# Kernel tuning notes

Hardware: AMD Instinct MI355X
Metric: run time of the kernel (lower is better)

The kernel has to match this reference:

```python
import jax, jax.numpy as jnp
import numpy as np

NEG = -9e15

def setup_inputs() -> dict:
    key = jax.random.key(0)
    k1, k2, k3, k4, k5 = jax.random.split(key, 5)
    N, Fin, Fout = 8192, 256, 128
    h = jax.random.normal(k1, (N, Fin), dtype=jnp.float32)
    adj = jax.random.randint(k2, (N, N), 0, 2, dtype=jnp.int32)
    # Parameters (xavier_uniform with gain=1.414 for a1/a2; kaiming-like for W is fine as random init)
    lim_w = float(np.sqrt(6.0 / (Fin + Fout)))
    W = jax.random.uniform(k3, (Fout, Fin), dtype=jnp.float32, minval=-lim_w, maxval=lim_w)
    lim_a = float(1.414 * np.sqrt(6.0 / (Fout + 1)))
    a1 = jax.random.uniform(k4, (Fout, 1), dtype=jnp.float32, minval=-lim_a, maxval=lim_a)
    a2 = jax.random.uniform(k5, (Fout, 1), dtype=jnp.float32, minval=-lim_a, maxval=lim_a)
    return {"h": h, "adj": adj, "W": W, "a1": a1, "a2": a2}

def reference(h, adj, W, a1, a2):
    Wh = h @ W.T                                   # [N, Fout]
    s1 = (Wh @ a1)                                 # [N, 1]
    s2 = (Wh @ a2)                                 # [N, 1]
    e = jax.nn.leaky_relu(s1 + s2.T, 0.2)          # [N, N]
    att = jnp.where(adj > 0, e, jnp.float32(NEG))
    att = jax.nn.softmax(att, axis=1)
    h_prime = att @ Wh                             # [N, Fout]
    return jax.nn.elu(h_prime)
```

## Files before the change

### kernel.cpp

```cpp
#include <hip/hip_runtime.h>
#include <cstdint>
#include <cstddef>

#define N_NODES 8192
#define FIN 256
#define FOUT 128
#define MT 32
#define KC 256
#define JS 4
#define JW (N_NODES / JS)
#define NCHS (JW / KC)
#define LOG2E 1.4426950408889634f

typedef __attribute__((ext_vector_type(8))) short bf16x8;
typedef __attribute__((ext_vector_type(4))) float f32x4;
typedef __attribute__((ext_vector_type(4))) int i32x4;
typedef __attribute__((ext_vector_type(2))) unsigned int u32x2;
typedef __attribute__((ext_vector_type(4))) unsigned int u32x4;

__device__ __forceinline__ float bf2f(unsigned short u) {
    union { unsigned int i; float f; } v; v.i = ((unsigned int)u) << 16; return v.f;
}
__device__ __forceinline__ unsigned short f2bf(float f) {
    union { float f; unsigned int i; } v; v.f = f;
    unsigned int r = (v.i + 0x7FFFu + ((v.i >> 16) & 1u)) >> 16;
    return (unsigned short)r;
}
__device__ __forceinline__ unsigned int pack_bf16(float a, float b) {
    return (unsigned)f2bf(a) | ((unsigned)f2bf(b) << 16);
}

__device__ __forceinline__ size_t whb_idx(int j, int f) {
    return ((size_t)((j >> 5) * 8 + (f >> 4)) << 9) + (((j >> 3) & 3) << 7)
         + ((f & 15) << 3) + (j & 7);
}

__global__ __launch_bounds__(256) void wh_kernel(const float* __restrict__ h,
                                                 const float* __restrict__ W,
                                                 const float* __restrict__ a1,
                                                 const float* __restrict__ a2,
                                                 unsigned short* __restrict__ whB,
                                                 float* __restrict__ s1p,
                                                 float* __restrict__ s2p) {
    __shared__ float hT[64][FIN + 5];
    __shared__ float p1[4][64], p2[4][64];
    const int t = threadIdx.x;
    const int i0 = blockIdx.x * 64;
    const int f0 = blockIdx.y * 32;
#pragma unroll
    for (int c = 0; c < 16; ++c) {
        int chunk = c * 256 + t;
        int row = chunk >> 6, col = (chunk & 63) * 4;
        f32x4 v = *(const f32x4*)&h[(size_t)(i0 + row) * FIN + col];
        hT[row][col] = v[0]; hT[row][col + 1] = v[1];
        hT[row][col + 2] = v[2]; hT[row][col + 3] = v[3];
    }
    __syncthreads();
    const int lane = t & 63;
    const int wv = t >> 6;
    const int fb8 = __builtin_amdgcn_readfirstlane(f0 + wv * 8);
    const float* w0 = W + (size_t)fb8 * FIN;
    float acc[8] = {0.f, 0.f, 0.f, 0.f, 0.f, 0.f, 0.f, 0.f};
    for (int k = 0; k < FIN; k += 4) {
        float h0 = hT[lane][k],     h1 = hT[lane][k + 1];
        float h2 = hT[lane][k + 2], h3 = hT[lane][k + 3];
#pragma unroll
        for (int c = 0; c < 8; ++c) {
            const float* wr = w0 + c * FIN;
            acc[c] += h0 * wr[k] + h1 * wr[k + 1] + h2 * wr[k + 2] + h3 * wr[k + 3];
        }
    }
    const int i = i0 + lane;
    float sp1 = 0.f, sp2 = 0.f;
#pragma unroll
    for (int c = 0; c < 8; ++c) {
        whB[whb_idx(i, fb8 + c)] = f2bf(acc[c]);
        sp1 += acc[c] * a1[fb8 + c];
        sp2 += acc[c] * a2[fb8 + c];
    }
    p1[wv][lane] = sp1; p2[wv][lane] = sp2;
    __syncthreads();
    if (t < 64) {
        float v1 = (p1[0][lane] + p1[1][lane]) + (p1[2][lane] + p1[3][lane]);
        float v2 = (p2[0][lane] + p2[1][lane]) + (p2[2][lane] + p2[3][lane]);
        s1p[(size_t)blockIdx.y * N_NODES + i0 + lane] = v1 * LOG2E;
        s2p[(size_t)blockIdx.y * N_NODES + i0 + lane] = v2 * LOG2E;
    }
}

__global__ __launch_bounds__(256) void gat_kernel(const int* __restrict__ adj,
                                                  const unsigned short* __restrict__ whB,
                                                  const float* __restrict__ s1p,
                                                  const float* __restrict__ s2p,
                                                  float* __restrict__ out,
                                                  float* __restrict__ nums,
                                                  float* __restrict__ dens) {
    __shared__ __align__(16) unsigned short sP[MT][KC + 8];
    __shared__ __align__(16) float sS2[JW / 1];
    __shared__ float sDen[MT];
    __shared__ float sS1[MT];
    const int t = threadIdx.x;
    const int slice = blockIdx.x & (JS - 1);
    const int i0 = (blockIdx.x >> 2) * MT;
    const int jb = slice * JW;
    const int kb0 = slice * (JW / 32);
    float* __restrict__ num = slice ? (nums + (size_t)(slice - 1) * N_NODES * FOUT) : out;
    float* __restrict__ den = dens + (size_t)slice * N_NODES;

    {
        const float* p0 = s2p + jb + t * 8;
        f32x4 a = {0.f, 0.f, 0.f, 0.f}, b = {0.f, 0.f, 0.f, 0.f};
#pragma unroll
        for (int pb = 0; pb < 4; ++pb) {
            a += *(const f32x4*)(p0 + (size_t)pb * N_NODES);
            b += *(const f32x4*)(p0 + (size_t)pb * N_NODES + 4);
        }
        *(f32x4*)&sS2[t * 8]     = a;
        *(f32x4*)&sS2[t * 8 + 4] = b;
    }
    if (t < MT) {
        float a = 0.f;
#pragma unroll
        for (int pb = 0; pb < 4; ++pb) a += s1p[(size_t)pb * N_NODES + i0 + t];
        sS1[t] = a;
        sDen[t] = 0.f;
    }
    __syncthreads();

    const int r0 = t >> 4;
    const int s  = t & 15;
    const int lane = t & 63;
    const int quad = lane >> 4;
    const int sl = lane & 15;
    const int wv = t >> 6;
    const int* __restrict__ aRow0 = adj + (size_t)(i0 + r0) * N_NODES + jb;
    const int* __restrict__ aRow1 = aRow0 + (size_t)16 * N_NODES;
    const float s1a = sS1[r0];
    const float s1b = sS1[r0 + 16];

    f32x4 acc00 = {0.f,0.f,0.f,0.f}, acc01 = {0.f,0.f,0.f,0.f};
    f32x4 acc10 = {0.f,0.f,0.f,0.f}, acc11 = {0.f,0.f,0.f,0.f};

    for (int ch = 0; ch < NCHS; ++ch) {
        const int cb = ch * KC + s * 16;
        i32x4 av0[4], av1[4];
        f32x4 sv[4];
#pragma unroll
        for (int q = 0; q < 4; ++q) {
            av0[q] = *(const i32x4*)&aRow0[cb + q * 4];
            av1[q] = *(const i32x4*)&aRow1[cb + q * 4];
            sv[q]  = *(const f32x4*)&sS2[cb + q * 4];
        }
        float part0 = 0.f, part1 = 0.f;
        unsigned int w0[8], w1[8];
#pragma unroll
        for (int q = 0; q < 4; ++q) {
            float p0[4], p1v[4];
#pragma unroll
            for (int r = 0; r < 4; ++r) {
                float y0 = s1a + sv[q][r];
                float y1 = s1b + sv[q][r];
                y0 = fmaxf(y0, 0.2f * y0);
                y1 = fmaxf(y1, 0.2f * y1);
                float e0 = __builtin_amdgcn_exp2f(y0);
                float e1 = __builtin_amdgcn_exp2f(y1);
                p0[r]  = (av0[q][r] > 0) ? e0 : 0.f;
                p1v[r] = (av1[q][r] > 0) ? e1 : 0.f;
                part0 += p0[r];
                part1 += p1v[r];
            }
            w0[2 * q]     = pack_bf16(p0[0], p0[1]);
            w0[2 * q + 1] = pack_bf16(p0[2], p0[3]);
            w1[2 * q]     = pack_bf16(p1v[0], p1v[1]);
            w1[2 * q + 1] = pack_bf16(p1v[2], p1v[3]);
        }
        u32x4 ra = {w0[0], w0[1], w0[2], w0[3]};
        u32x4 rb = {w0[4], w0[5], w0[6], w0[7]};
        u32x4 rc = {w1[0], w1[1], w1[2], w1[3]};
        u32x4 rd = {w1[4], w1[5], w1[6], w1[7]};
        *(u32x4*)&sP[r0][s * 16]          = ra;
        *(u32x4*)&sP[r0][s * 16 + 8]      = rb;
        *(u32x4*)&sP[r0 + 16][s * 16]     = rc;
        *(u32x4*)&sP[r0 + 16][s * 16 + 8] = rd;
        part0 += __shfl_xor(part0, 1); part1 += __shfl_xor(part1, 1);
        part0 += __shfl_xor(part0, 2); part1 += __shfl_xor(part1, 2);
        part0 += __shfl_xor(part0, 4); part1 += __shfl_xor(part1, 4);
        part0 += __shfl_xor(part0, 8); part1 += __shfl_xor(part1, 8);
        if (s == 0) { sDen[r0] += part0; sDen[r0 + 16] += part1; }
        __syncthreads();
#pragma unroll
        for (int kq = 0; kq < KC / 32; ++kq) {
            bf16x8 a0  = *(const bf16x8*)&sP[sl][kq * 32 + quad * 8];
            bf16x8 a1f = *(const bf16x8*)&sP[16 + sl][kq * 32 + quad * 8];
            int kb = kb0 + ch * (KC / 32) + kq;
            const unsigned short* t0 = whB + ((size_t)(kb * 8 + wv * 2) << 9) + lane * 8;
            bf16x8 b0 = *(const bf16x8*)t0;
            bf16x8 b1 = *(const bf16x8*)(t0 + 512);
            acc00 = __builtin_amdgcn_mfma_f32_16x16x32_bf16(a0,  b0, acc00, 0, 0, 0);
            acc01 = __builtin_amdgcn_mfma_f32_16x16x32_bf16(a0,  b1, acc01, 0, 0, 0);
            acc10 = __builtin_amdgcn_mfma_f32_16x16x32_bf16(a1f, b0, acc10, 0, 0, 0);
            acc11 = __builtin_amdgcn_mfma_f32_16x16x32_bf16(a1f, b1, acc11, 0, 0, 0);
        }
        __syncthreads();
    }
    if (t < MT) den[i0 + t] = sDen[t];
#pragma unroll
    for (int m = 0; m < 2; ++m) {
#pragma unroll
        for (int nn = 0; nn < 2; ++nn) {
            f32x4 a = (m == 0) ? (nn == 0 ? acc00 : acc01) : (nn == 0 ? acc10 : acc11);
#pragma unroll
            for (int r = 0; r < 4; ++r) {
                int row = m * 16 + quad * 4 + r;
                num[(size_t)(i0 + row) * FOUT + wv * 32 + nn * 16 + sl] = a[r];
            }
        }
    }
}

__global__ __launch_bounds__(256) void fin_kernel(float* __restrict__ out,
                                                  const float* __restrict__ nums,
                                                  const float* __restrict__ dens) {
    const int idx4 = blockIdx.x * 256 + threadIdx.x;
    const int idx = idx4 * 4;
    const int i = idx >> 7;
    const size_t NF = (size_t)N_NODES * FOUT;
    f32x4 n0 = *(f32x4*)&out[idx];
    f32x4 n1 = *(const f32x4*)&nums[idx];
    f32x4 n2 = *(const f32x4*)&nums[NF + idx];
    f32x4 n3 = *(const f32x4*)&nums[2 * NF + idx];
    float denv = dens[i] + dens[N_NODES + i] + dens[2 * N_NODES + i] + dens[3 * N_NODES + i];
    float dv = fmaxf(denv, 1e-30f);
    f32x4 r;
#pragma unroll
    for (int k = 0; k < 4; ++k) {
        float numv = (n0[k] + n1[k]) + (n2[k] + n3[k]);
        float v = numv / dv;
        r[k] = (v > 0.f) ? v : expm1f(v);
    }
    *(f32x4*)&out[idx] = r;
}

extern "C" void kernel_launch(void* const* d_in, const int* in_sizes, int n_in,
                              void* d_out, int out_size, void* d_ws, size_t ws_size,
                              hipStream_t stream) {
    const float* h   = (const float*)d_in[0];
    const int*   adj = (const int*)d_in[1];
    const float* W   = (const float*)d_in[2];
    const float* a1  = (const float*)d_in[3];
    const float* a2  = (const float*)d_in[4];

    char* ws = (char*)d_ws;
    unsigned short* whB = (unsigned short*)ws;
    float* s1p  = (float*)(ws + (4u << 20));
    float* s2p  = s1p + 4 * N_NODES;
    float* dens = s2p + 4 * N_NODES;
    float* nums = dens + 4 * N_NODES;
    float* out  = (float*)d_out;

    wh_kernel<<<dim3(N_NODES / 64, FOUT / 32), 256, 0, stream>>>(h, W, a1, a2,
                                                                 whB, s1p, s2p);
    gat_kernel<<<dim3((N_NODES / MT) * JS), 256, 0, stream>>>(adj, whB, s1p, s2p,
                                                              out, nums, dens);
    fin_kernel<<<dim3(N_NODES * FOUT / 1024), 256, 0, stream>>>(out, nums, dens);
}
```

Before: 399.3 us.

## Compute Wh projection with bf16 MFMA and stream adjacency with nontemporal loads

Rewrites the h·Wᵀ projection kernel to use bf16 16x16x32 MFMA instructions. W is packed to bf16 in LDS and h rows are read directly from global memory, replacing the scalar FP32 loop over a transposed LDS tile. The attention score partials are now reduced with cross-lane shuffles instead of a shared-memory pass. The main attention kernel also loads the int32 adjacency matrix with nontemporal hints to limit cache pollution. Quantising h and W to bf16 before the projection lowers the precision of Wh, s1 and s2.

```diff
diff --git a/kernel.cpp b/kernel.cpp
--- a/kernel.cpp
+++ b/kernel.cpp
@@ -42,49 +42,69 @@
                                                  unsigned short* __restrict__ whB,
                                                  float* __restrict__ s1p,
                                                  float* __restrict__ s2p) {
-    __shared__ float hT[64][FIN + 5];
-    __shared__ float p1[4][64], p2[4][64];
+    __shared__ __align__(16) unsigned short wLds[16 * 64 * 8];
     const int t = threadIdx.x;
     const int i0 = blockIdx.x * 64;
     const int f0 = blockIdx.y * 32;
-#pragma unroll
-    for (int c = 0; c < 16; ++c) {
-        int chunk = c * 256 + t;
-        int row = chunk >> 6, col = (chunk & 63) * 4;
-        f32x4 v = *(const f32x4*)&h[(size_t)(i0 + row) * FIN + col];
-        hT[row][col] = v[0]; hT[row][col + 1] = v[1];
-        hT[row][col + 2] = v[2]; hT[row][col + 3] = v[3];
+    {
+        const int kk = t & 7;
+        const int fr = t >> 3;
+        const int fh = fr >> 4;
+        const float* wr = W + (size_t)(f0 + fr) * FIN + kk * 32;
+#pragma unroll
+        for (int g = 0; g < 4; ++g) {
+            f32x4 v0 = *(const f32x4*)(wr + g * 8);
+            f32x4 v1 = *(const f32x4*)(wr + g * 8 + 4);
+            u32x4 pk;
+            pk.x = pack_bf16(v0[0], v0[1]); pk.y = pack_bf16(v0[2], v0[3]);
+            pk.z = pack_bf16(v1[0], v1[1]); pk.w = pack_bf16(v1[2], v1[3]);
+            *(u32x4*)&wLds[(size_t)(((kk * 2 + fh) * 64) + (fr & 15) + g * 16) * 8] = pk;
+        }
     }
     __syncthreads();
     const int lane = t & 63;
     const int wv = t >> 6;
-    const int fb8 = __builtin_amdgcn_readfirstlane(f0 + wv * 8);
-    const float* w0 = W + (size_t)fb8 * FIN;
-    float acc[8] = {0.f, 0.f, 0.f, 0.f, 0.f, 0.f, 0.f, 0.f};
-    for (int k = 0; k < FIN; k += 4) {
-        float h0 = hT[lane][k],     h1 = hT[lane][k + 1];
-        float h2 = hT[lane][k + 2], h3 = hT[lane][k + 3];
-#pragma unroll
-        for (int c = 0; c < 8; ++c) {
-            const float* wr = w0 + c * FIN;
-            acc[c] += h0 * wr[k] + h1 * wr[k + 1] + h2 * wr[k + 2] + h3 * wr[k + 3];
-        }
-    }
-    const int i = i0 + lane;
-    float sp1 = 0.f, sp2 = 0.f;
-#pragma unroll
-    for (int c = 0; c < 8; ++c) {
-        whB[whb_idx(i, fb8 + c)] = f2bf(acc[c]);
-        sp1 += acc[c] * a1[fb8 + c];
-        sp2 += acc[c] * a2[fb8 + c];
-    }
-    p1[wv][lane] = sp1; p2[wv][lane] = sp2;
-    __syncthreads();
-    if (t < 64) {
-        float v1 = (p1[0][lane] + p1[1][lane]) + (p1[2][lane] + p1[3][lane]);
-        float v2 = (p2[0][lane] + p2[1][lane]) + (p2[2][lane] + p2[3][lane]);
-        s1p[(size_t)blockIdx.y * N_NODES + i0 + lane] = v1 * LOG2E;
-        s2p[(size_t)blockIdx.y * N_NODES + i0 + lane] = v2 * LOG2E;
+    const int quad = lane >> 4;
+    const int sl = lane & 15;
+    const float* hRow = h + (size_t)(i0 + wv * 16 + sl) * FIN + quad * 8;
+    f32x4 acc0 = {0.f,0.f,0.f,0.f}, acc1 = {0.f,0.f,0.f,0.f};
+#pragma unroll
+    for (int kk = 0; kk < 8; ++kk) {
+        f32x4 v0 = *(const f32x4*)(hRow + kk * 32);
+        f32x4 v1 = *(const f32x4*)(hRow + kk * 32 + 4);
+        union { u32x4 u; bf16x8 b; } A;
+        A.u.x = pack_bf16(v0[0], v0[1]); A.u.y = pack_bf16(v0[2], v0[3]);
+        A.u.z = pack_bf16(v1[0], v1[1]); A.u.w = pack_bf16(v1[2], v1[3]);
+        bf16x8 B0 = *(const bf16x8*)&wLds[(size_t)((kk * 2 + 0) * 64 + lane) * 8];
+        bf16x8 B1 = *(const bf16x8*)&wLds[(size_t)((kk * 2 + 1) * 64 + lane) * 8];
+        acc0 = __builtin_amdgcn_mfma_f32_16x16x32_bf16(A.b, B0, acc0, 0, 0, 0);
+        acc1 = __builtin_amdgcn_mfma_f32_16x16x32_bf16(A.b, B1, acc1, 0, 0, 0);
+    }
+    const float a1v0 = a1[f0 + sl], a1v1 = a1[f0 + 16 + sl];
+    const float a2v0 = a2[f0 + sl], a2v1 = a2[f0 + 16 + sl];
+    float c1[4], c2[4];
+#pragma unroll
+    for (int r = 0; r < 4; ++r) {
+        int i = i0 + wv * 16 + quad * 4 + r;
+        whB[whb_idx(i, f0 + sl)]      = f2bf(acc0[r]);
+        whB[whb_idx(i, f0 + 16 + sl)] = f2bf(acc1[r]);
+        c1[r] = acc0[r] * a1v0 + acc1[r] * a1v1;
+        c2[r] = acc0[r] * a2v0 + acc1[r] * a2v1;
+    }
+#pragma unroll
+    for (int r = 0; r < 4; ++r) {
+        c1[r] += __shfl_xor(c1[r], 1); c2[r] += __shfl_xor(c2[r], 1);
+        c1[r] += __shfl_xor(c1[r], 2); c2[r] += __shfl_xor(c2[r], 2);
+        c1[r] += __shfl_xor(c1[r], 4); c2[r] += __shfl_xor(c2[r], 4);
+        c1[r] += __shfl_xor(c1[r], 8); c2[r] += __shfl_xor(c2[r], 8);
+    }
+    if (sl == 0) {
+#pragma unroll
+        for (int r = 0; r < 4; ++r) {
+            int i = i0 + wv * 16 + quad * 4 + r;
+            s1p[(size_t)blockIdx.y * N_NODES + i] = c1[r] * LOG2E;
+            s2p[(size_t)blockIdx.y * N_NODES + i] = c2[r] * LOG2E;
+        }
     }
 }
 
@@ -96,7 +116,7 @@
                                                   float* __restrict__ nums,
                                                   float* __restrict__ dens) {
     __shared__ __align__(16) unsigned short sP[MT][KC + 8];
-    __shared__ __align__(16) float sS2[JW / 1];
+    __shared__ __align__(16) float sS2[JW];
     __shared__ float sDen[MT];
     __shared__ float sS1[MT];
     const int t = threadIdx.x;
@@ -147,8 +167,8 @@
         f32x4 sv[4];
 #pragma unroll
         for (int q = 0; q < 4; ++q) {
-            av0[q] = *(const i32x4*)&aRow0[cb + q * 4];
-            av1[q] = *(const i32x4*)&aRow1[cb + q * 4];
+            av0[q] = __builtin_nontemporal_load((const i32x4*)&aRow0[cb + q * 4]);
+            av1[q] = __builtin_nontemporal_load((const i32x4*)&aRow1[cb + q * 4]);
             sv[q]  = *(const f32x4*)&sS2[cb + q * 4];
         }
         float part0 = 0.f, part1 = 0.f;
```

Measured after the change: 421.0 us. 1.05x slower.
